# Performance work log

Measured on AMD Instinct MI355X. Metric: run time of the kernel, lower is better.

Reference implementation:

```python
import jax, jax.numpy as jnp
import numpy as np
from jax import lax

N = 2048
NUM_CLASSES = 21  # background + 20 classes


def xy_to_cxcy(xy):
    return jnp.concatenate([(xy[:, 2:] + xy[:, :2]) / 2.0, xy[:, 2:] - xy[:, :2]], axis=-1)


def cxcy_to_xy(c):
    return jnp.concatenate([c[:, :2] - c[:, 2:] / 2.0, c[:, :2] + c[:, 2:] / 2.0], axis=-1)


def gcxgcy_to_cxcy(g, priors_cxcy):
    # offsets already pre-scaled (/10, /20) by the caller, matching the torch forward
    return jnp.concatenate([g[:, :2] * priors_cxcy[:, 2:] + priors_cxcy[:, :2],
                            jnp.exp(g[:, 2:]) * priors_cxcy[:, 2:]], axis=-1)


def pairwise_iou(a, b):
    # a: [N,4], b: [M,4] corner format -> [N,M]
    lt = jnp.maximum(a[:, None, :2], b[None, :, :2])
    rb = jnp.minimum(a[:, None, 2:], b[None, :, 2:])
    wh = jnp.clip(rb - lt, 0.0)
    inter = wh[..., 0] * wh[..., 1]
    area_a = (a[:, 2] - a[:, 0]) * (a[:, 3] - a[:, 1])
    area_b = (b[:, 2] - b[:, 0]) * (b[:, 3] - b[:, 1])
    return inter / (area_a[:, None] + area_b[None, :] - inter)


def _detect(rois_xy, predicted_locs, predicted_scores, min_score, max_overlap, top_k):
    n = rois_xy.shape[0]
    rois_cxcy = xy_to_cxcy(rois_xy)
    locs = predicted_locs.reshape(n, -1, 4)                      # [N, C, 4]
    probs = jax.nn.softmax(predicted_scores, axis=1)             # [N, C]
    best = jnp.argmax(probs, axis=1)                             # locs for argmax class
    g = jnp.take_along_axis(locs, best[:, None, None], axis=1)[:, 0, :]
    g = jnp.concatenate([g[:, :2] / 10.0, g[:, 2:] / 20.0], axis=-1)
    decoded = cxcy_to_xy(gcxgcy_to_cxcy(g, rois_cxcy))           # [N, 4]

    def nms_class(cls_scores):
        valid = cls_scores > min_score
        s = jnp.where(valid, cls_scores, -jnp.inf)
        order = jnp.argsort(-s)                                  # desc; invalid last
        s_sorted = s[order]
        b_sorted = decoded[order]
        ov = lax.stop_gradient(pairwise_iou(b_sorted, b_sorted))  # [N, N]
        sup0 = ~valid[order]                                     # invalid start suppressed

        def body(i, sup):
            new = jnp.logical_or(sup, ov[i] > max_overlap)
            new = new.at[i].set(False)                           # never self-suppress
            return jnp.where(sup[i], sup, new)                   # skip already-suppressed

        sup = lax.fori_loop(0, n, body, sup0)
        return b_sorted, jnp.where(~sup, s_sorted, -jnp.inf)

    # vmap the greedy NMS over the 20 foreground classes
    boxes_c, scores_c = jax.vmap(nms_class)(probs[:, 1:].T)      # [20,N,4], [20,N]
    labels_c = jnp.broadcast_to(jnp.arange(1, NUM_CLASSES)[:, None], scores_c.shape)

    fs = scores_c.reshape(-1)
    fb = boxes_c.reshape(-1, 4)
    fl = labels_c.reshape(-1)
    topv, topi = lax.top_k(fs, top_k)
    ok = jnp.isfinite(topv)
    out_boxes = jnp.where(ok[:, None], fb[topi],
                          jnp.array([0.0, 0.0, 1.0, 1.0], dtype=fb.dtype))
    out_labels = jnp.where(ok, fl[topi], 0)
    out_scores = jnp.where(ok, topv, 0.0)
    return out_boxes, out_labels, out_scores


def setup_inputs() -> dict:
    key = jax.random.key(0)
    k1, k2, k3, k4 = jax.random.split(key, 4)
    cxcy = jax.random.uniform(k1, (N, 2), minval=0.1, maxval=0.9)
    wh = jax.random.uniform(k2, (N, 2), minval=0.05, maxval=0.3)
    rois_xy = jnp.concatenate([cxcy - wh / 2.0, cxcy + wh / 2.0], axis=-1)
    predicted_locs = jax.random.normal(k3, (N, NUM_CLASSES * 4), dtype=jnp.float32) * 0.5
    predicted_scores = jax.random.normal(k4, (N, NUM_CLASSES), dtype=jnp.float32) * 2.0
    return {"rois_xy": rois_xy,
            "predicted_locs": predicted_locs,
            "predicted_scores": predicted_scores,
            "min_score": jnp.float32(0.01),
            "max_overlap": jnp.float32(0.45),
            "top_k": 100}


def reference(rois_xy, predicted_locs, predicted_scores, min_score, max_overlap, top_k):
    return _detect(rois_xy, predicted_locs, predicted_scores, min_score, max_overlap, top_k)
```

## Files before the change

### kernel.cpp

```cpp
#include <hip/hip_runtime.h>
#include <cstdint>

#define NROI 2048
#define NCLS 21
#define NFG  20
#define CPAD 128
#define CTOT (NFG * CPAD)
#define NTHR 1024
#define SBLK 256
#define RSEL 480
#define SCAP 512
#define CSEL 512
#define DROWS 64
#define INVH 0xFF800000u

typedef unsigned long long u64;
typedef unsigned int u32;

__device__ __forceinline__ u32 desc_key(float s) {
  u32 u = __float_as_uint(s);
  u32 asc = (u & 0x80000000u) ? ~u : (u | 0x80000000u);
  return ~asc;
}
__device__ __forceinline__ float key_to_float(u32 desc) {
  u32 asc = ~desc;
  u32 u = (asc & 0x80000000u) ? (asc ^ 0x80000000u) : ~asc;
  return __uint_as_float(u);
}
__device__ __forceinline__ u64 shflx_u64(u64 v, int m) {
  u32 lo = (u32)v, hi = (u32)(v >> 32);
  lo = (u32)__shfl_xor((int)lo, m);
  hi = (u32)__shfl_xor((int)hi, m);
  return ((u64)hi << 32) | (u64)lo;
}
__device__ __forceinline__ void cmpex64(u64& mine, u64 other, int i, int j, int k) {
  bool amIlow = ((i & j) == 0);
  bool dir = ((i & k) == 0);
  bool otherLess = other < mine;
  if (otherLess != (amIlow != dir)) mine = other;
}

__device__ __forceinline__ void bucket_select(const int* h, int need, int lane,
                                              int* outB, int* outC) {
  int base = lane << 2;
  int c0 = h[base], c1 = h[base + 1], c2 = h[base + 2], c3 = h[base + 3];
  int s = c0 + c1 + c2 + c3;
  int pre = s;
  #pragma unroll
  for (int off = 1; off < 64; off <<= 1) {
    int v = __shfl_up(pre, off);
    if (lane >= off) pre += v;
  }
  u64 ball = __ballot(pre >= need);
  int ln = __ffsll((long long)ball) - 1;
  int exc = __shfl(pre, ln) - __shfl(s, ln);
  int b0 = __shfl(c0, ln), b1 = __shfl(c1, ln), b2 = __shfl(c2, ln);
  int bkt, cb;
  if (exc + b0 >= need)                { bkt = (ln << 2) + 0; cb = exc; }
  else if (exc + b0 + b1 >= need)      { bkt = (ln << 2) + 1; cb = exc + b0; }
  else if (exc + b0 + b1 + b2 >= need) { bkt = (ln << 2) + 2; cb = exc + b0 + b1; }
  else                                 { bkt = (ln << 2) + 3; cb = exc + b0 + b1 + b2; }
  if (lane == 0) { *outB = bkt; *outC = cb; }
}

__global__ __launch_bounds__(64)
void k_decode(const float* __restrict__ rois,
              const float* __restrict__ locs,
              const float* __restrict__ scores,
              float* __restrict__ probsT,
              float4* __restrict__ decoded,
              u32* __restrict__ done) {
  __shared__ float srow[DROWS][NCLS + 2];
  const int tid = threadIdx.x;
  const int rbase = blockIdx.x * DROWS;
  if (rbase == 0 && tid == 0) *done = 0u;

  const float* src = scores + (size_t)rbase * NCLS;
  for (int t = tid; t < DROWS * NCLS; t += 64)
    srow[t / NCLS][t % NCLS] = src[t];
  __syncthreads();

  const int r = rbase + tid;
  float s[NCLS];
  #pragma unroll
  for (int c = 0; c < NCLS; ++c) s[c] = srow[tid][c];
  float m = s[0];
  #pragma unroll
  for (int c = 0; c < NCLS; ++c) m = fmaxf(m, s[c]);
  float sum = 0.0f;
  #pragma unroll
  for (int c = 0; c < NCLS; ++c) { s[c] = expf(s[c] - m); sum += s[c]; }

  float pb = s[0] / sum; int best = 0;
  #pragma unroll
  for (int c = 1; c < NCLS; ++c) {
    float p = s[c] / sum;
    probsT[(c - 1) * NROI + r] = p;
    if (p > pb) { pb = p; best = c; }
  }

  float4 roi = ((const float4*)rois)[r];
  float pcx = __fmul_rn(__fadd_rn(roi.x, roi.z), 0.5f);
  float pcy = __fmul_rn(__fadd_rn(roi.y, roi.w), 0.5f);
  float pw  = __fsub_rn(roi.z, roi.x);
  float ph  = __fsub_rn(roi.w, roi.y);

  float4 gl = ((const float4*)locs)[r * NCLS + best];
  float g0 = gl.x / 10.0f;
  float g1 = gl.y / 10.0f;
  float g2 = gl.z / 20.0f;
  float g3 = gl.w / 20.0f;

  float cx = __fadd_rn(__fmul_rn(g0, pw), pcx);
  float cy = __fadd_rn(__fmul_rn(g1, ph), pcy);
  float w  = __fmul_rn(expf(g2), pw);
  float h  = __fmul_rn(expf(g3), ph);
  float hw = __fmul_rn(w, 0.5f);
  float hh = __fmul_rn(h, 0.5f);
  decoded[r] = make_float4(__fsub_rn(cx, hw), __fsub_rn(cy, hh),
                           __fadd_rn(cx, hw), __fadd_rn(cy, hh));
}

__global__ __launch_bounds__(NTHR)
void k_nms(const float* __restrict__ probsT,
           const float4* __restrict__ decoded,
           const float* __restrict__ min_score_p,
           const float* __restrict__ max_overlap_p,
           u64* __restrict__ cand,
           float4* __restrict__ cbox,
           u32* __restrict__ done,
           float* __restrict__ out,
           const int* __restrict__ top_k_p) {
  __shared__ u32 LDSW[7296];
  __shared__ u64 remInitW[4];
  __shared__ int hist1[256], hist2[256];
  __shared__ int cntLds, scLds, cSelSh, selB1, selC1, selB2, selD2, mSh, cCnt;
  __shared__ u32 lastSh;

  u64* mbAu    = (u64*)(LDSW + 0);
  u64* mbBu    = (u64*)(LDSW + 1024);
  u64* skeyW64 = (u64*)(LDSW + 2048);
  u64* maskW   = (u64*)(LDSW + 3072);
  float* bx0   = (float*)(LDSW + 5120);
  float* by0   = (float*)(LDSW + 5376);
  float* bx1   = (float*)(LDSW + 5632);
  float* by1   = (float*)(LDSW + 5888);
  float* areaA = (float*)(LDSW + 6144);
  float* sx0   = (float*)(LDSW + 6400);
  float* sy0   = (float*)(LDSW + 6528);
  float* sx1   = (float*)(LDSW + 6656);
  float* sy1   = (float*)(LDSW + 6784);
  float* sarea = (float*)(LDSW + 6912);
  u32* survKeyH = LDSW + 7040;
  u32* survRows = LDSW + 7168;

  const int cls = blockIdx.x;
  const int tid = threadIdx.x;
  const int lane = tid & 63;
  const int wid = tid >> 6;
  const float msc = *min_score_p;
  const float ovr = *max_overlap_p;
  const int K = *top_k_p;
  const int Kcap = (K < CPAD) ? K : CPAD;

  if (tid == 0) { cntLds = 0; scLds = 0; }
  __syncthreads();

  float p0v = probsT[cls * NROI + tid];
  float p1v = probsT[cls * NROI + tid + 1024];
  bool v0 = p0v > msc, v1 = p1v > msc;
  u64 kq0 = ((u64)desc_key(v0 ? p0v : -__builtin_inff()) << 32) | (u32)tid;
  u64 kq1 = ((u64)desc_key(v1 ? p1v : -__builtin_inff()) << 32) | (u32)(tid + 1024);
  {
    u64 ba = __ballot(v0), bb = __ballot(v1);
    if (lane == 0) atomicAdd(&cntLds, __popcll(ba) + __popcll(bb));
  }
  __syncthreads();
  const int nv = cntLds;

  int sc = 0;
  int processed = 0;
  u64 minKey = 0ULL;

  while (sc < Kcap && processed < nv) {
    int rem = nv - processed;
    int need = (rem < RSEL) ? rem : RSEL;

    if (tid < 256) { hist1[tid] = 0; hist2[tid] = 0; }
    if (tid == 0) cSelSh = 0;
    __syncthreads();
    bool val0 = (kq0 > minKey) && ((u32)(kq0 >> 32) < INVH);
    bool val1 = (kq1 > minKey) && ((u32)(kq1 >> 32) < INVH);
    if (val0) atomicAdd(&hist1[(int)((kq0 >> 56) & 255)], 1);
    if (val1) atomicAdd(&hist1[(int)((kq1 >> 56) & 255)], 1);
    __syncthreads();
    if (wid == 0) bucket_select(hist1, need, lane, &selB1, &selC1);
    __syncthreads();
    const int B1 = selB1, C1 = selC1;
    if (val0 && (int)((kq0 >> 56) & 255) == B1)
      atomicAdd(&hist2[(int)((kq0 >> 48) & 255)], 1);
    if (val1 && (int)((kq1 >> 56) & 255) == B1)
      atomicAdd(&hist2[(int)((kq1 >> 48) & 255)], 1);
    __syncthreads();
    if (wid == 0) bucket_select(hist2, need - C1, lane, &selB2, &selD2);
    __syncthreads();
    const int pred16 = (selB1 << 8) | selB2;

    bool s0 = val0 && (int)((kq0 >> 48) & 0xFFFF) <= pred16;
    bool s1 = val1 && (int)((kq1 >> 48) & 0xFFFF) <= pred16;
    {
      u64 b0 = __ballot(s0), b1 = __ballot(s1);
      int cnt = __popcll(b0) + __popcll(b1);
      int basePos = 0;
      if (lane == 0) basePos = cnt ? atomicAdd(&cSelSh, cnt) : 0;
      basePos = __shfl(basePos, 0);
      u64 lm = (1ULL << lane) - 1ULL;
      int p0 = basePos + __popcll(b0 & lm);
      int p1 = basePos + __popcll(b0) + __popcll(b1 & lm);
      if (s0 && p0 < SCAP) mbAu[p0] = kq0;
      if (s1 && p1 < SCAP) mbAu[p1] = kq1;
    }
    __syncthreads();
    int Csel = cSelSh; if (Csel > SCAP) Csel = SCAP;
    if (tid < SCAP && tid >= Csel) mbAu[tid] = ~0ULL;
    __syncthreads();

    u64 key = (tid < SCAP) ? mbAu[tid] : ~0ULL;
    int parity = 0;
    auto ldsp = [&](int k, int j) {
      u64* buf = parity ? mbBu : mbAu; parity ^= 1;
      if (tid < SCAP) buf[tid] = key;
      __syncthreads();
      if (tid < SCAP) { u64 o = buf[tid ^ j]; cmpex64(key, o, tid, j, k); }
    };
    auto shfp = [&](int k, int j) {
      if (tid < SCAP) { u64 o = shflx_u64(key, j); cmpex64(key, o, tid, j, k); }
    };
    for (int k = 2; k <= 64; k <<= 1)
      for (int j = k >> 1; j >= 1; j >>= 1) shfp(k, j);
    ldsp(128, 64);
    for (int j = 32; j >= 1; j >>= 1) shfp(128, j);
    ldsp(256, 128); ldsp(256, 64);
    for (int j = 32; j >= 1; j >>= 1) shfp(256, j);
    ldsp(512, 256); ldsp(512, 128); ldsp(512, 64);
    for (int j = 32; j >= 1; j >>= 1) shfp(512, j);
    if (tid < SCAP) skeyW64[tid] = key;
    __syncthreads();

    for (int base = 0; base < Csel && sc < Kcap; base += SBLK) {
      int RL = Csel - base; if (RL > SBLK) RL = SBLK;
      if (tid < SBLK) {
        int p = base + tid; if (p > Csel - 1) p = Csel - 1;
        u64 kq = skeyW64[p];
        float4 b = decoded[(u32)kq];
        bx0[tid] = b.x; by0[tid] = b.y; bx1[tid] = b.z; by1[tid] = b.w;
        areaA[tid] = __fmul_rn(__fsub_rn(b.z, b.x), __fsub_rn(b.w, b.y));
      }
      if (tid < 4) remInitW[tid] = 0ULL;
      __syncthreads();

      if (sc > 0 && tid < SBLK) {
        float jx0 = bx0[tid], jy0 = by0[tid], jx1 = bx1[tid], jy1 = by1[tid];
        float ab = areaA[tid];
        bool kill = false;
        for (int u = 0; u < sc; ++u) {
          float ix0 = sx0[u], iy0 = sy0[u], ix1 = sx1[u], iy1 = sy1[u];
          float ia = sarea[u];
          float lx = fmaxf(ix0, jx0), ly = fmaxf(iy0, jy0);
          float rx = fminf(ix1, jx1), ry = fminf(iy1, jy1);
          float w_ = fmaxf(__fsub_rn(rx, lx), 0.0f);
          float h_ = fmaxf(__fsub_rn(ry, ly), 0.0f);
          float inter = __fmul_rn(w_, h_);
          float iou = __fdiv_rn(inter, __fsub_rn(__fadd_rn(ia, ab), inter));
          kill = kill || (iou > ovr);
        }
        u64 bal = __ballot(kill);
        if (lane == 0) remInitW[wid] = bal;
      }
      __syncthreads();

      {
        int nw = (RL + 63) >> 6;
        for (int r2 = wid; r2 < RL; r2 += 16) {
          if ((remInitW[r2 >> 6] >> (r2 & 63)) & 1ULL) continue;
          float ix0 = bx0[r2], iy0 = by0[r2], ix1 = bx1[r2], iy1 = by1[r2];
          float ia = areaA[r2];
          for (int ct = (r2 >> 6); ct < nw; ++ct) {
            int j = (ct << 6) + lane;
            float jx0 = bx0[j], jy0 = by0[j], jx1 = bx1[j], jy1 = by1[j];
            float ab = areaA[j];
            float lx = fmaxf(ix0, jx0), ly = fmaxf(iy0, jy0);
            float rx = fminf(ix1, jx1), ry = fminf(iy1, jy1);
            float w_ = fmaxf(__fsub_rn(rx, lx), 0.0f);
            float h_ = fmaxf(__fsub_rn(ry, ly), 0.0f);
            float inter = __fmul_rn(w_, h_);
            float iou = __fdiv_rn(inter, __fsub_rn(__fadd_rn(ia, ab), inter));
            bool bit = iou > ovr;
            if (ct == (r2 >> 6)) bit = bit && (j > r2);
            u64 bal = __ballot(bit);
            if (lane == 0) maskW[(r2 << 2) + ct] = bal;
          }
        }
      }
      __syncthreads();

      if (wid == 0) {
        int t0 = RL;
        u64 rw0 = (t0 <= 0) ? ~0ULL : ((t0 >= 64) ? 0ULL : (~0ULL << t0));
        int t1 = t0 - 64;
        u64 rw1 = (t1 <= 0) ? ~0ULL : ((t1 >= 64) ? 0ULL : (~0ULL << t1));
        int t2 = t0 - 128;
        u64 rw2 = (t2 <= 0) ? ~0ULL : ((t2 >= 64) ? 0ULL : (~0ULL << t2));
        int t3 = t0 - 192;
        u64 rw3 = (t3 <= 0) ? ~0ULL : ((t3 >= 64) ? 0ULL : (~0ULL << t3));
        rw0 |= remInitW[0]; rw1 |= remInitW[1];
        rw2 |= remInitW[2]; rw3 |= remInitW[3];
        int scW = sc;
        bool full = scW >= Kcap;
        u64 a00,a01,a02,a03,a10,a11,a12,a13,a20,a21,a22,a23,a30,a31,a32,a33;
        u64 b00,b01,b02,b03,b10,b11,b12,b13,b20,b21,b22,b23,b30,b31,b32,b33;
#define LD4(V0,V1,V2,V3,R) { int rr_ = (R); \
        V0 = maskW[(rr_<<2)+0]; V1 = maskW[(rr_<<2)+1]; \
        V2 = maskW[(rr_<<2)+2]; V3 = maskW[(rr_<<2)+3]; }
#define PRX(RWG, BIT, M0,M1,M2,M3, ROW) \
        if (!full && !(((RWG) >> (BIT)) & 1ULL)) { \
          rw0 |= (M0); rw1 |= (M1); rw2 |= (M2); rw3 |= (M3); \
          if (lane == 0) survRows[scW] = (u32)(base + (ROW)); \
          ++scW; full = (scW >= Kcap); \
        }
#define SWEEPG(G, RWG) \
        if (!full && (((G) << 6) < RL)) { \
          const int rb = (G) << 6; \
          LD4(a00,a01,a02,a03, rb+0) LD4(a10,a11,a12,a13, rb+1) \
          LD4(a20,a21,a22,a23, rb+2) LD4(a30,a31,a32,a33, rb+3) \
          for (int bb = 0; bb < 64 && !full; bb += 4) { \
            LD4(b00,b01,b02,b03, rb+bb+4) LD4(b10,b11,b12,b13, rb+bb+5) \
            LD4(b20,b21,b22,b23, rb+bb+6) LD4(b30,b31,b32,b33, rb+bb+7) \
            PRX(RWG, bb+0, a00,a01,a02,a03, rb+bb+0) \
            PRX(RWG, bb+1, a10,a11,a12,a13, rb+bb+1) \
            PRX(RWG, bb+2, a20,a21,a22,a23, rb+bb+2) \
            PRX(RWG, bb+3, a30,a31,a32,a33, rb+bb+3) \
            a00=b00;a01=b01;a02=b02;a03=b03; a10=b10;a11=b11;a12=b12;a13=b13; \
            a20=b20;a21=b21;a22=b22;a23=b23; a30=b30;a31=b31;a32=b32;a33=b33; \
          } \
        }
        SWEEPG(0, rw0) SWEEPG(1, rw1) SWEEPG(2, rw2) SWEEPG(3, rw3)
#undef SWEEPG
#undef PRX
#undef LD4
        if (lane == 0) scLds = scW;
      }
      __syncthreads();

      {
        int scNew = scLds;
        if (tid >= sc && tid < scNew) {
          int wrow = (int)survRows[tid];
          int rr = wrow - base;
          sx0[tid] = bx0[rr]; sy0[tid] = by0[rr];
          sx1[tid] = bx1[rr]; sy1[tid] = by1[rr];
          sarea[tid] = areaA[rr];
          survKeyH[tid] = (u32)(skeyW64[wrow] >> 32);
        }
        __syncthreads();
        sc = scNew;
      }
    }

    minKey = skeyW64[Csel - 1];
    processed += Csel;
    __syncthreads();
  }

  if (tid < CPAD) {
    int o = cls * CPAD + tid;
    if (tid < sc) {
      cand[o] = ((u64)survKeyH[tid] << 32) | (u32)o;
      cbox[o] = make_float4(sx0[tid], sy0[tid], sx1[tid], sy1[tid]);
    } else {
      cand[o] = ~0ULL;
    }
  }

  __threadfence();
  __syncthreads();
  if (tid == 0) lastSh = atomicAdd(done, 1u);
  __syncthreads();
  if (lastSh != NFG - 1) return;
  __threadfence();

  u64* kk = (u64*)LDSW;
  u64* ck = (u64*)(LDSW + 5120);
  if (tid == 0) cCnt = 0;
  if (tid < 256) { hist1[tid] = 0; hist2[tid] = 0; }
  __syncthreads();
  for (int t = tid; t < CTOT; t += NTHR) {
    u64 v = cand[t];
    kk[t] = v;
    if (v != ~0ULL) atomicAdd(&hist1[(int)(v >> 56)], 1);
  }
  __syncthreads();
  if (wid == 0) {
    int b4 = lane << 2;
    int s = hist1[b4] + hist1[b4 + 1] + hist1[b4 + 2] + hist1[b4 + 3];
    #pragma unroll
    for (int off = 32; off; off >>= 1) s += __shfl_xor(s, off);
    if (lane == 0) mSh = s;
  }
  __syncthreads();
  const int M = mSh;
  const int Kneed = (K < M) ? K : M;

  if (Kneed > 0) {
    if (wid == 0) bucket_select(hist1, Kneed, lane, &selB1, &selC1);
    __syncthreads();
    const int B1 = selB1, C1 = selC1;
    for (int t = tid; t < CTOT; t += NTHR) {
      u64 v = kk[t];
      if (v != ~0ULL && (int)(v >> 56) == B1)
        atomicAdd(&hist2[(int)((v >> 48) & 255)], 1);
    }
    __syncthreads();
    if (wid == 0) bucket_select(hist2, Kneed - C1, lane, &selB2, &selD2);
    __syncthreads();
    const int B2 = selB2;
    for (int t = tid; t < CTOT; t += NTHR) {
      u64 v = kk[t];
      if (v == ~0ULL) continue;
      int b1 = (int)(v >> 56);
      int b2 = (int)((v >> 48) & 255);
      if (b1 < B1 || (b1 == B1 && b2 <= B2)) {
        int pos = atomicAdd(&cCnt, 1);
        if (pos < CSEL) ck[pos] = v;
      }
    }
    __syncthreads();
    const int C = cCnt;
    if (C <= CSEL) {
      if (tid < C) {
        u64 my = ck[tid];
        int rank = 0;
        for (int u = 0; u < C; ++u) rank += (ck[u] < my) ? 1 : 0;
        if (rank < K) {
          u32 flat = (u32)(my & 0xFFFFFFFFu);
          float score = key_to_float((u32)(my >> 32));
          int c2 = (int)(flat >> 7);
          float4 b = cbox[flat];
          out[rank * 4 + 0] = b.x;
          out[rank * 4 + 1] = b.y;
          out[rank * 4 + 2] = b.z;
          out[rank * 4 + 3] = b.w;
          out[K * 4 + rank] = (float)(c2 + 1);
          out[K * 5 + rank] = score;
        }
      }
    } else {
      for (int t = tid; t < CTOT; t += NTHR) {
        u64 kap = kk[t];
        if (kap == ~0ULL) continue;
        int rank = 0;
        #pragma unroll
        for (int cc2 = 0; cc2 < NFG; ++cc2) {
          const u64* a = kk + cc2 * CPAD;
          int lb = 0;
          #pragma unroll
          for (int s2 = CPAD >> 1; s2; s2 >>= 1) {
            int pq = lb + s2;
            if (a[pq - 1] < kap) lb = pq;
          }
          rank += lb;
        }
        if (rank < K) {
          u32 flat = (u32)(kap & 0xFFFFFFFFu);
          float score = key_to_float((u32)(kap >> 32));
          int c2 = (int)(flat >> 7);
          float4 b = cbox[flat];
          out[rank * 4 + 0] = b.x;
          out[rank * 4 + 1] = b.y;
          out[rank * 4 + 2] = b.z;
          out[rank * 4 + 3] = b.w;
          out[K * 4 + rank] = (float)(c2 + 1);
          out[K * 5 + rank] = score;
        }
      }
    }
  }
  __syncthreads();
  for (int r = tid; r < K; r += NTHR) {
    if (r >= M) {
      out[r * 4 + 0] = 0.0f; out[r * 4 + 1] = 0.0f;
      out[r * 4 + 2] = 1.0f; out[r * 4 + 3] = 1.0f;
      out[K * 4 + r] = 0.0f;
      out[K * 5 + r] = 0.0f;
    }
  }
}

extern "C" void kernel_launch(void* const* d_in, const int* in_sizes, int n_in,
                              void* d_out, int out_size, void* d_ws, size_t ws_size,
                              hipStream_t stream) {
  const float* rois        = (const float*)d_in[0];
  const float* locs        = (const float*)d_in[1];
  const float* scores      = (const float*)d_in[2];
  const float* min_score   = (const float*)d_in[3];
  const float* max_overlap = (const float*)d_in[4];
  const int*   top_k       = (const int*)d_in[5];

  char* ws = (char*)d_ws;
  u64*    cand    = (u64*)ws;
  float4* cbox    = (float4*)(ws + 20480);
  float*  probsT  = (float*)(ws + 20480 + 40960);
  float4* decoded = (float4*)(ws + 20480 + 40960 + 163840);
  u32*    done    = (u32*)(ws + 20480 + 40960 + 163840 + 32768);

  k_decode<<<NROI / DROWS, 64, 0, stream>>>(rois, locs, scores, probsT, decoded, done);
  k_nms<<<NFG, NTHR, 0, stream>>>(probsT, decoded, min_score, max_overlap,
                                  cand, cbox, done, (float*)d_out, top_k);
}
```

Measured before the change: 58.08 us.

## Fuse softmax and box decode into NMS kernel, drop separate decode launch

Removes the separate decode kernel. Each NMS block now computes the softmax for its own class over all rows by staging the score matrix through LDS in chunks. It decodes boxes only for the selected candidates, straight into shared memory. This removes one kernel launch and the probsT/decoded global round trips. In exchange every block redoes the full softmax over all 2048 rows and adds a memset launch to reset the done counter.

```diff
diff --git a/kernel.cpp b/kernel.cpp
--- a/kernel.cpp
+++ b/kernel.cpp
@@ -11,7 +11,6 @@
 #define RSEL 480
 #define SCAP 512
 #define CSEL 512
-#define DROWS 64
 #define INVH 0xFF800000u
 
 typedef unsigned long long u64;
@@ -63,67 +62,10 @@
   if (lane == 0) { *outB = bkt; *outC = cb; }
 }
 
-__global__ __launch_bounds__(64)
-void k_decode(const float* __restrict__ rois,
-              const float* __restrict__ locs,
-              const float* __restrict__ scores,
-              float* __restrict__ probsT,
-              float4* __restrict__ decoded,
-              u32* __restrict__ done) {
-  __shared__ float srow[DROWS][NCLS + 2];
-  const int tid = threadIdx.x;
-  const int rbase = blockIdx.x * DROWS;
-  if (rbase == 0 && tid == 0) *done = 0u;
-
-  const float* src = scores + (size_t)rbase * NCLS;
-  for (int t = tid; t < DROWS * NCLS; t += 64)
-    srow[t / NCLS][t % NCLS] = src[t];
-  __syncthreads();
-
-  const int r = rbase + tid;
-  float s[NCLS];
-  #pragma unroll
-  for (int c = 0; c < NCLS; ++c) s[c] = srow[tid][c];
-  float m = s[0];
-  #pragma unroll
-  for (int c = 0; c < NCLS; ++c) m = fmaxf(m, s[c]);
-  float sum = 0.0f;
-  #pragma unroll
-  for (int c = 0; c < NCLS; ++c) { s[c] = expf(s[c] - m); sum += s[c]; }
-
-  float pb = s[0] / sum; int best = 0;
-  #pragma unroll
-  for (int c = 1; c < NCLS; ++c) {
-    float p = s[c] / sum;
-    probsT[(c - 1) * NROI + r] = p;
-    if (p > pb) { pb = p; best = c; }
-  }
-
-  float4 roi = ((const float4*)rois)[r];
-  float pcx = __fmul_rn(__fadd_rn(roi.x, roi.z), 0.5f);
-  float pcy = __fmul_rn(__fadd_rn(roi.y, roi.w), 0.5f);
-  float pw  = __fsub_rn(roi.z, roi.x);
-  float ph  = __fsub_rn(roi.w, roi.y);
-
-  float4 gl = ((const float4*)locs)[r * NCLS + best];
-  float g0 = gl.x / 10.0f;
-  float g1 = gl.y / 10.0f;
-  float g2 = gl.z / 20.0f;
-  float g3 = gl.w / 20.0f;
-
-  float cx = __fadd_rn(__fmul_rn(g0, pw), pcx);
-  float cy = __fadd_rn(__fmul_rn(g1, ph), pcy);
-  float w  = __fmul_rn(expf(g2), pw);
-  float h  = __fmul_rn(expf(g3), ph);
-  float hw = __fmul_rn(w, 0.5f);
-  float hh = __fmul_rn(h, 0.5f);
-  decoded[r] = make_float4(__fsub_rn(cx, hw), __fsub_rn(cy, hh),
-                           __fadd_rn(cx, hw), __fadd_rn(cy, hh));
-}
-
 __global__ __launch_bounds__(NTHR)
-void k_nms(const float* __restrict__ probsT,
-           const float4* __restrict__ decoded,
+void k_nms(const float* __restrict__ rois,
+           const float* __restrict__ locs,
+           const float* __restrict__ scores,
            const float* __restrict__ min_score_p,
            const float* __restrict__ max_overlap_p,
            u64* __restrict__ cand,
@@ -131,7 +73,7 @@
            u32* __restrict__ done,
            float* __restrict__ out,
            const int* __restrict__ top_k_p) {
-  __shared__ u32 LDSW[7296];
+  __shared__ u32 LDSW[12800];
   __shared__ u64 remInitW[4];
   __shared__ int hist1[256], hist2[256];
   __shared__ int cntLds, scLds, cSelSh, selB1, selC1, selB2, selD2, mSh, cCnt;
@@ -153,8 +95,15 @@
   float* sarea = (float*)(LDSW + 6912);
   u32* survKeyH = LDSW + 7040;
   u32* survRows = LDSW + 7168;
+  float* wx0 = (float*)(LDSW + 7296);
+  float* wy0 = (float*)(LDSW + 7808);
+  float* wx1 = (float*)(LDSW + 8320);
+  float* wy1 = (float*)(LDSW + 8832);
+  float* stgF  = (float*)LDSW;
+  u32* keyCol  = LDSW + 10752;
 
   const int cls = blockIdx.x;
+  const int cc = cls + 1;
   const int tid = threadIdx.x;
   const int lane = tid & 63;
   const int wid = tid >> 6;
@@ -164,15 +113,36 @@
   const int Kcap = (K < CPAD) ? K : CPAD;
 
   if (tid == 0) { cntLds = 0; scLds = 0; }
-  __syncthreads();
-
-  float p0v = probsT[cls * NROI + tid];
-  float p1v = probsT[cls * NROI + tid + 1024];
-  bool v0 = p0v > msc, v1 = p1v > msc;
-  u64 kq0 = ((u64)desc_key(v0 ? p0v : -__builtin_inff()) << 32) | (u32)tid;
-  u64 kq1 = ((u64)desc_key(v1 ? p1v : -__builtin_inff()) << 32) | (u32)(tid + 1024);
+
+  for (int chunk = 0; chunk < 4; ++chunk) {
+    const float* src = scores + (size_t)chunk * 512 * NCLS;
+    for (int t = tid; t < 512 * NCLS; t += NTHR) stgF[t] = src[t];
+    __syncthreads();
+    if (tid < 512) {
+      const float* row = stgF + tid * NCLS;
+      float s[NCLS];
+      #pragma unroll
+      for (int c = 0; c < NCLS; ++c) s[c] = row[c];
+      float m = s[0];
+      #pragma unroll
+      for (int c = 0; c < NCLS; ++c) m = fmaxf(m, s[c]);
+      float sum = 0.0f;
+      #pragma unroll
+      for (int c = 0; c < NCLS; ++c) { s[c] = expf(s[c] - m); sum += s[c]; }
+      float ec = s[0];
+      #pragma unroll
+      for (int c = 1; c < NCLS; ++c) ec = (c == cc) ? s[c] : ec;
+      float p = ec / sum;
+      keyCol[chunk * 512 + tid] = desc_key((p > msc) ? p : -__builtin_inff());
+    }
+    __syncthreads();
+  }
+
+  u32 h0k = keyCol[tid], h1k = keyCol[tid + 1024];
+  u64 kq0 = ((u64)h0k << 32) | (u32)tid;
+  u64 kq1 = ((u64)h1k << 32) | (u32)(tid + 1024);
   {
-    u64 ba = __ballot(v0), bb = __ballot(v1);
+    u64 ba = __ballot(h0k < INVH), bb = __ballot(h1k < INVH);
     if (lane == 0) atomicAdd(&cntLds, __popcll(ba) + __popcll(bb));
   }
   __syncthreads();
@@ -245,16 +215,55 @@
     ldsp(512, 256); ldsp(512, 128); ldsp(512, 64);
     for (int j = 32; j >= 1; j >>= 1) shfp(512, j);
     if (tid < SCAP) skeyW64[tid] = key;
+
+    if (tid < SCAP && tid < Csel) {
+      int row = (int)(u32)key;
+      const float* sr = scores + row * NCLS;
+      float s[NCLS];
+      #pragma unroll
+      for (int c = 0; c < NCLS; ++c) s[c] = sr[c];
+      float m = s[0];
+      #pragma unroll
+      for (int c = 0; c < NCLS; ++c) m = fmaxf(m, s[c]);
+      float sum = 0.0f;
+      #pragma unroll
+      for (int c = 0; c < NCLS; ++c) { s[c] = expf(s[c] - m); sum += s[c]; }
+      float pb = s[0] / sum; int best = 0;
+      #pragma unroll
+      for (int c = 1; c < NCLS; ++c) {
+        float p = s[c] / sum;
+        if (p > pb) { pb = p; best = c; }
+      }
+      float4 roi = ((const float4*)rois)[row];
+      float pcx = __fmul_rn(__fadd_rn(roi.x, roi.z), 0.5f);
+      float pcy = __fmul_rn(__fadd_rn(roi.y, roi.w), 0.5f);
+      float pw  = __fsub_rn(roi.z, roi.x);
+      float ph  = __fsub_rn(roi.w, roi.y);
+      float4 gl = ((const float4*)locs)[row * NCLS + best];
+      float g0 = gl.x / 10.0f;
+      float g1 = gl.y / 10.0f;
+      float g2 = gl.z / 20.0f;
+      float g3 = gl.w / 20.0f;
+      float cx = __fadd_rn(__fmul_rn(g0, pw), pcx);
+      float cy = __fadd_rn(__fmul_rn(g1, ph), pcy);
+      float w  = __fmul_rn(expf(g2), pw);
+      float h  = __fmul_rn(expf(g3), ph);
+      float hw = __fmul_rn(w, 0.5f);
+      float hh = __fmul_rn(h, 0.5f);
+      wx0[tid] = __fsub_rn(cx, hw);
+      wy0[tid] = __fsub_rn(cy, hh);
+      wx1[tid] = __fadd_rn(cx, hw);
+      wy1[tid] = __fadd_rn(cy, hh);
+    }
     __syncthreads();
 
     for (int base = 0; base < Csel && sc < Kcap; base += SBLK) {
       int RL = Csel - base; if (RL > SBLK) RL = SBLK;
       if (tid < SBLK) {
         int p = base + tid; if (p > Csel - 1) p = Csel - 1;
-        u64 kq = skeyW64[p];
-        float4 b = decoded[(u32)kq];
-        bx0[tid] = b.x; by0[tid] = b.y; bx1[tid] = b.z; by1[tid] = b.w;
-        areaA[tid] = __fmul_rn(__fsub_rn(b.z, b.x), __fsub_rn(b.w, b.y));
+        float x0v = wx0[p], y0v = wy0[p], x1v = wx1[p], y1v = wy1[p];
+        bx0[tid] = x0v; by0[tid] = y0v; bx1[tid] = x1v; by1[tid] = y1v;
+        areaA[tid] = __fmul_rn(__fsub_rn(x1v, x0v), __fsub_rn(y1v, y0v));
       }
       if (tid < 4) remInitW[tid] = 0ULL;
       __syncthreads();
@@ -507,13 +516,11 @@
   const int*   top_k       = (const int*)d_in[5];
 
   char* ws = (char*)d_ws;
-  u64*    cand    = (u64*)ws;
-  float4* cbox    = (float4*)(ws + 20480);
-  float*  probsT  = (float*)(ws + 20480 + 40960);
-  float4* decoded = (float4*)(ws + 20480 + 40960 + 163840);
-  u32*    done    = (u32*)(ws + 20480 + 40960 + 163840 + 32768);
-
-  k_decode<<<NROI / DROWS, 64, 0, stream>>>(rois, locs, scores, probsT, decoded, done);
-  k_nms<<<NFG, NTHR, 0, stream>>>(probsT, decoded, min_score, max_overlap,
+  u64*    cand = (u64*)ws;
+  float4* cbox = (float4*)(ws + 20480);
+  u32*    done = (u32*)(ws + 20480 + 40960);
+
+  hipMemsetAsync(done, 0, 4, stream);
+  k_nms<<<NFG, NTHR, 0, stream>>>(rois, locs, scores, min_score, max_overlap,
                                   cand, cbox, done, (float*)d_out, top_k);
 }
```

Result: slower. 71.01 us (+22.3%).

## Overlap second-block IoU mask build with first-block serial sweep in NMS

Applied to the files above, without the earlier changes.

Replaces the loop over 256-candidate blocks with two explicit blocks held in separate LDS buffers. Both blocks' boxes are loaded together. The second block's pairwise suppression mask is computed by waves 1-15 while wave 0 runs the serial greedy sweep over the first block. The first block's kill check against prior survivors is folded into its box load, which saves a barrier. This costs extra LDS and skips the early exit before computing the second mask, so that mask is built even when the first block already fills top-k.

```diff
diff --git a/kernel.cpp b/kernel.cpp
--- a/kernel.cpp
+++ b/kernel.cpp
@@ -131,7 +131,7 @@
            u32* __restrict__ done,
            float* __restrict__ out,
            const int* __restrict__ top_k_p) {
-  __shared__ u32 LDSW[7296];
+  __shared__ u32 LDSW[10624];
   __shared__ u64 remInitW[4];
   __shared__ int hist1[256], hist2[256];
   __shared__ int cntLds, scLds, cSelSh, selB1, selC1, selB2, selD2, mSh, cCnt;
@@ -153,6 +153,12 @@
   float* sarea = (float*)(LDSW + 6912);
   u32* survKeyH = LDSW + 7040;
   u32* survRows = LDSW + 7168;
+  float* bx0B  = (float*)(LDSW + 7296);
+  float* by0B  = (float*)(LDSW + 7552);
+  float* bx1B  = (float*)(LDSW + 7808);
+  float* by1B  = (float*)(LDSW + 8064);
+  float* areaB = (float*)(LDSW + 8320);
+  u64* maskWB  = (u64*)(LDSW + 8576);
 
   const int cls = blockIdx.x;
   const int tid = threadIdx.x;
@@ -181,6 +187,53 @@
   int sc = 0;
   int processed = 0;
   u64 minKey = 0ULL;
+
+  auto sweep = [&](const u64* MW, int RL, int sbase) {
+    int t0 = RL;
+    u64 rw0 = (t0 <= 0) ? ~0ULL : ((t0 >= 64) ? 0ULL : (~0ULL << t0));
+    int t1 = t0 - 64;
+    u64 rw1 = (t1 <= 0) ? ~0ULL : ((t1 >= 64) ? 0ULL : (~0ULL << t1));
+    int t2 = t0 - 128;
+    u64 rw2 = (t2 <= 0) ? ~0ULL : ((t2 >= 64) ? 0ULL : (~0ULL << t2));
+    int t3 = t0 - 192;
+    u64 rw3 = (t3 <= 0) ? ~0ULL : ((t3 >= 64) ? 0ULL : (~0ULL << t3));
+    rw0 |= remInitW[0]; rw1 |= remInitW[1];
+    rw2 |= remInitW[2]; rw3 |= remInitW[3];
+    int scW = sc;
+    bool full = scW >= Kcap;
+    u64 a00,a01,a02,a03,a10,a11,a12,a13,a20,a21,a22,a23,a30,a31,a32,a33;
+    u64 b00,b01,b02,b03,b10,b11,b12,b13,b20,b21,b22,b23,b30,b31,b32,b33;
+#define LD4(V0,V1,V2,V3,R) { int rr_ = (R); \
+    V0 = MW[(rr_<<2)+0]; V1 = MW[(rr_<<2)+1]; \
+    V2 = MW[(rr_<<2)+2]; V3 = MW[(rr_<<2)+3]; }
+#define PRX(RWG, BIT, M0,M1,M2,M3, ROW) \
+    if (!full && !(((RWG) >> (BIT)) & 1ULL)) { \
+      rw0 |= (M0); rw1 |= (M1); rw2 |= (M2); rw3 |= (M3); \
+      if (lane == 0) survRows[scW] = (u32)(sbase + (ROW)); \
+      ++scW; full = (scW >= Kcap); \
+    }
+#define SWEEPG(G, RWG) \
+    if (!full && (((G) << 6) < RL)) { \
+      const int rb = (G) << 6; \
+      LD4(a00,a01,a02,a03, rb+0) LD4(a10,a11,a12,a13, rb+1) \
+      LD4(a20,a21,a22,a23, rb+2) LD4(a30,a31,a32,a33, rb+3) \
+      for (int bb = 0; bb < 64 && !full; bb += 4) { \
+        LD4(b00,b01,b02,b03, rb+bb+4) LD4(b10,b11,b12,b13, rb+bb+5) \
+        LD4(b20,b21,b22,b23, rb+bb+6) LD4(b30,b31,b32,b33, rb+bb+7) \
+        PRX(RWG, bb+0, a00,a01,a02,a03, rb+bb+0) \
+        PRX(RWG, bb+1, a10,a11,a12,a13, rb+bb+1) \
+        PRX(RWG, bb+2, a20,a21,a22,a23, rb+bb+2) \
+        PRX(RWG, bb+3, a30,a31,a32,a33, rb+bb+3) \
+        a00=b00;a01=b01;a02=b02;a03=b03; a10=b10;a11=b11;a12=b12;a13=b13; \
+        a20=b20;a21=b21;a22=b22;a23=b23; a30=b30;a31=b31;a32=b32;a33=b33; \
+      } \
+    }
+    SWEEPG(0, rw0) SWEEPG(1, rw1) SWEEPG(2, rw2) SWEEPG(3, rw3)
+#undef SWEEPG
+#undef PRX
+#undef LD4
+    if (lane == 0) scLds = scW;
+  };
 
   while (sc < Kcap && processed < nv) {
     int rem = nv - processed;
@@ -247,119 +300,137 @@
     if (tid < SCAP) skeyW64[tid] = key;
     __syncthreads();
 
-    for (int base = 0; base < Csel && sc < Kcap; base += SBLK) {
-      int RL = Csel - base; if (RL > SBLK) RL = SBLK;
-      if (tid < SBLK) {
-        int p = base + tid; if (p > Csel - 1) p = Csel - 1;
-        u64 kq = skeyW64[p];
-        float4 b = decoded[(u32)kq];
-        bx0[tid] = b.x; by0[tid] = b.y; bx1[tid] = b.z; by1[tid] = b.w;
-        areaA[tid] = __fmul_rn(__fsub_rn(b.z, b.x), __fsub_rn(b.w, b.y));
-      }
-      if (tid < 4) remInitW[tid] = 0ULL;
-      __syncthreads();
-
-      if (sc > 0 && tid < SBLK) {
-        float jx0 = bx0[tid], jy0 = by0[tid], jx1 = bx1[tid], jy1 = by1[tid];
-        float ab = areaA[tid];
-        bool kill = false;
-        for (int u = 0; u < sc; ++u) {
-          float ix0 = sx0[u], iy0 = sy0[u], ix1 = sx1[u], iy1 = sy1[u];
-          float ia = sarea[u];
+    const int RL1 = (Csel < SBLK) ? Csel : SBLK;
+    const int RL2 = Csel - RL1;
+
+    if (tid < SBLK) {
+      int p = tid; if (p > Csel - 1) p = Csel - 1;
+      u64 kq = skeyW64[p];
+      float4 b = decoded[(u32)kq];
+      bx0[tid] = b.x; by0[tid] = b.y; bx1[tid] = b.z; by1[tid] = b.w;
+      float ab = __fmul_rn(__fsub_rn(b.z, b.x), __fsub_rn(b.w, b.y));
+      areaA[tid] = ab;
+      bool kill = false;
+      for (int u = 0; u < sc; ++u) {
+        float ix0 = sx0[u], iy0 = sy0[u], ix1 = sx1[u], iy1 = sy1[u];
+        float ia = sarea[u];
+        float lx = fmaxf(ix0, b.x), ly = fmaxf(iy0, b.y);
+        float rx = fminf(ix1, b.z), ry = fminf(iy1, b.w);
+        float w_ = fmaxf(__fsub_rn(rx, lx), 0.0f);
+        float h_ = fmaxf(__fsub_rn(ry, ly), 0.0f);
+        float inter = __fmul_rn(w_, h_);
+        float iou = __fdiv_rn(inter, __fsub_rn(__fadd_rn(ia, ab), inter));
+        kill = kill || (iou > ovr);
+      }
+      u64 bal = __ballot(kill);
+      if (lane == 0) remInitW[wid] = bal;
+    } else if (tid < 2 * SBLK && RL2 > 0) {
+      int p = tid; if (p > Csel - 1) p = Csel - 1;
+      u64 kq = skeyW64[p];
+      float4 b = decoded[(u32)kq];
+      int t2 = tid - SBLK;
+      bx0B[t2] = b.x; by0B[t2] = b.y; bx1B[t2] = b.z; by1B[t2] = b.w;
+      areaB[t2] = __fmul_rn(__fsub_rn(b.z, b.x), __fsub_rn(b.w, b.y));
+    }
+    __syncthreads();
+
+    {
+      int nw = (RL1 + 63) >> 6;
+      for (int r2 = wid; r2 < RL1; r2 += 16) {
+        if ((remInitW[r2 >> 6] >> (r2 & 63)) & 1ULL) continue;
+        float ix0 = bx0[r2], iy0 = by0[r2], ix1 = bx1[r2], iy1 = by1[r2];
+        float ia = areaA[r2];
+        for (int ct = (r2 >> 6); ct < nw; ++ct) {
+          int j = (ct << 6) + lane;
+          float jx0 = bx0[j], jy0 = by0[j], jx1 = bx1[j], jy1 = by1[j];
+          float ab = areaA[j];
           float lx = fmaxf(ix0, jx0), ly = fmaxf(iy0, jy0);
           float rx = fminf(ix1, jx1), ry = fminf(iy1, jy1);
           float w_ = fmaxf(__fsub_rn(rx, lx), 0.0f);
           float h_ = fmaxf(__fsub_rn(ry, ly), 0.0f);
           float inter = __fmul_rn(w_, h_);
           float iou = __fdiv_rn(inter, __fsub_rn(__fadd_rn(ia, ab), inter));
-          kill = kill || (iou > ovr);
-        }
-        u64 bal = __ballot(kill);
-        if (lane == 0) remInitW[wid] = bal;
+          bool bit = iou > ovr;
+          if (ct == (r2 >> 6)) bit = bit && (j > r2);
+          u64 bal = __ballot(bit);
+          if (lane == 0) maskW[(r2 << 2) + ct] = bal;
+        }
+      }
+    }
+    __syncthreads();
+
+    if (wid == 0) {
+      sweep(maskW, RL1, 0);
+    } else if (RL2 > 0) {
+      int nw2 = (RL2 + 63) >> 6;
+      for (int r2 = wid - 1; r2 < RL2; r2 += 15) {
+        float ix0 = bx0B[r2], iy0 = by0B[r2], ix1 = bx1B[r2], iy1 = by1B[r2];
+        float ia = areaB[r2];
+        for (int ct = (r2 >> 6); ct < nw2; ++ct) {
+          int j = (ct << 6) + lane;
+          float jx0 = bx0B[j], jy0 = by0B[j], jx1 = bx1B[j], jy1 = by1B[j];
+          float ab = areaB[j];
+          float lx = fmaxf(ix0, jx0), ly = fmaxf(iy0, jy0);
+          float rx = fminf(ix1, jx1), ry = fminf(iy1, jy1);
+          float w_ = fmaxf(__fsub_rn(rx, lx), 0.0f);
+          float h_ = fmaxf(__fsub_rn(ry, ly), 0.0f);
+          float inter = __fmul_rn(w_, h_);
+          float iou = __fdiv_rn(inter, __fsub_rn(__fadd_rn(ia, ab), inter));
+          bool bit = iou > ovr;
+          if (ct == (r2 >> 6)) bit = bit && (j > r2);
+          u64 bal = __ballot(bit);
+          if (lane == 0) maskWB[(r2 << 2) + ct] = bal;
+        }
+      }
+    }
+    __syncthreads();
+
+    {
+      int scNew = scLds;
+      if (tid >= sc && tid < scNew) {
+        int wrow = (int)survRows[tid];
+        sx0[tid] = bx0[wrow]; sy0[tid] = by0[wrow];
+        sx1[tid] = bx1[wrow]; sy1[tid] = by1[wrow];
+        sarea[tid] = areaA[wrow];
+        survKeyH[tid] = (u32)(skeyW64[wrow] >> 32);
       }
       __syncthreads();
-
-      {
-        int nw = (RL + 63) >> 6;
-        for (int r2 = wid; r2 < RL; r2 += 16) {
-          if ((remInitW[r2 >> 6] >> (r2 & 63)) & 1ULL) continue;
-          float ix0 = bx0[r2], iy0 = by0[r2], ix1 = bx1[r2], iy1 = by1[r2];
-          float ia = areaA[r2];
-          for (int ct = (r2 >> 6); ct < nw; ++ct) {
-            int j = (ct << 6) + lane;
-            float jx0 = bx0[j], jy0 = by0[j], jx1 = bx1[j], jy1 = by1[j];
-            float ab = areaA[j];
+      sc = scNew;
+    }
+
+    if (sc < Kcap && RL2 > 0) {
+      if (tid < SBLK) {
+        bool kill = false;
+        if (tid < RL2) {
+          float jx0 = bx0B[tid], jy0 = by0B[tid];
+          float jx1 = bx1B[tid], jy1 = by1B[tid];
+          float ab = areaB[tid];
+          for (int u = 0; u < sc; ++u) {
+            float ix0 = sx0[u], iy0 = sy0[u], ix1 = sx1[u], iy1 = sy1[u];
+            float ia = sarea[u];
             float lx = fmaxf(ix0, jx0), ly = fmaxf(iy0, jy0);
             float rx = fminf(ix1, jx1), ry = fminf(iy1, jy1);
             float w_ = fmaxf(__fsub_rn(rx, lx), 0.0f);
             float h_ = fmaxf(__fsub_rn(ry, ly), 0.0f);
             float inter = __fmul_rn(w_, h_);
             float iou = __fdiv_rn(inter, __fsub_rn(__fadd_rn(ia, ab), inter));
-            bool bit = iou > ovr;
-            if (ct == (r2 >> 6)) bit = bit && (j > r2);
-            u64 bal = __ballot(bit);
-            if (lane == 0) maskW[(r2 << 2) + ct] = bal;
+            kill = kill || (iou > ovr);
           }
         }
+        u64 bal = __ballot(kill);
+        if (lane == 0) remInitW[wid] = bal;
       }
       __syncthreads();
-
-      if (wid == 0) {
-        int t0 = RL;
-        u64 rw0 = (t0 <= 0) ? ~0ULL : ((t0 >= 64) ? 0ULL : (~0ULL << t0));
-        int t1 = t0 - 64;
-        u64 rw1 = (t1 <= 0) ? ~0ULL : ((t1 >= 64) ? 0ULL : (~0ULL << t1));
-        int t2 = t0 - 128;
-        u64 rw2 = (t2 <= 0) ? ~0ULL : ((t2 >= 64) ? 0ULL : (~0ULL << t2));
-        int t3 = t0 - 192;
-        u64 rw3 = (t3 <= 0) ? ~0ULL : ((t3 >= 64) ? 0ULL : (~0ULL << t3));
-        rw0 |= remInitW[0]; rw1 |= remInitW[1];
-        rw2 |= remInitW[2]; rw3 |= remInitW[3];
-        int scW = sc;
-        bool full = scW >= Kcap;
-        u64 a00,a01,a02,a03,a10,a11,a12,a13,a20,a21,a22,a23,a30,a31,a32,a33;
-        u64 b00,b01,b02,b03,b10,b11,b12,b13,b20,b21,b22,b23,b30,b31,b32,b33;
-#define LD4(V0,V1,V2,V3,R) { int rr_ = (R); \
-        V0 = maskW[(rr_<<2)+0]; V1 = maskW[(rr_<<2)+1]; \
-        V2 = maskW[(rr_<<2)+2]; V3 = maskW[(rr_<<2)+3]; }
-#define PRX(RWG, BIT, M0,M1,M2,M3, ROW) \
-        if (!full && !(((RWG) >> (BIT)) & 1ULL)) { \
-          rw0 |= (M0); rw1 |= (M1); rw2 |= (M2); rw3 |= (M3); \
-          if (lane == 0) survRows[scW] = (u32)(base + (ROW)); \
-          ++scW; full = (scW >= Kcap); \
-        }
-#define SWEEPG(G, RWG) \
-        if (!full && (((G) << 6) < RL)) { \
-          const int rb = (G) << 6; \
-          LD4(a00,a01,a02,a03, rb+0) LD4(a10,a11,a12,a13, rb+1) \
-          LD4(a20,a21,a22,a23, rb+2) LD4(a30,a31,a32,a33, rb+3) \
-          for (int bb = 0; bb < 64 && !full; bb += 4) { \
-            LD4(b00,b01,b02,b03, rb+bb+4) LD4(b10,b11,b12,b13, rb+bb+5) \
-            LD4(b20,b21,b22,b23, rb+bb+6) LD4(b30,b31,b32,b33, rb+bb+7) \
-            PRX(RWG, bb+0, a00,a01,a02,a03, rb+bb+0) \
-            PRX(RWG, bb+1, a10,a11,a12,a13, rb+bb+1) \
-            PRX(RWG, bb+2, a20,a21,a22,a23, rb+bb+2) \
-            PRX(RWG, bb+3, a30,a31,a32,a33, rb+bb+3) \
-            a00=b00;a01=b01;a02=b02;a03=b03; a10=b10;a11=b11;a12=b12;a13=b13; \
-            a20=b20;a21=b21;a22=b22;a23=b23; a30=b30;a31=b31;a32=b32;a33=b33; \
-          } \
-        }
-        SWEEPG(0, rw0) SWEEPG(1, rw1) SWEEPG(2, rw2) SWEEPG(3, rw3)
-#undef SWEEPG
-#undef PRX
-#undef LD4
-        if (lane == 0) scLds = scW;
-      }
+      if (wid == 0) sweep(maskWB, RL2, SBLK);
       __syncthreads();
-
       {
         int scNew = scLds;
         if (tid >= sc && tid < scNew) {
           int wrow = (int)survRows[tid];
-          int rr = wrow - base;
-          sx0[tid] = bx0[rr]; sy0[tid] = by0[rr];
-          sx1[tid] = bx1[rr]; sy1[tid] = by1[rr];
-          sarea[tid] = areaA[rr];
+          int rr = wrow - SBLK;
+          sx0[tid] = bx0B[rr]; sy0[tid] = by0B[rr];
+          sx1[tid] = bx1B[rr]; sy1[tid] = by1B[rr];
+          sarea[tid] = areaB[rr];
           survKeyH[tid] = (u32)(skeyW64[wrow] >> 32);
         }
         __syncthreads();
```

After: 59.61 us. 1.03x slower.
